# Performance work log

Hardware: AMD Instinct MI355X
Metric: run time of the kernel (lower is better)

Reference implementation:

```python
import jax, jax.numpy as jnp
import numpy as np

W_CHAMFER = 1.0
W_SMOOTH = 0.5
K_NEIGHBORS = 8


def _pairwise_sqdist(a, b):
    # a: [B,N,3], b: [B,M,3] -> [B,N,M] squared euclidean distances
    a2 = jnp.sum(a * a, axis=-1)  # [B,N]
    b2 = jnp.sum(b * b, axis=-1)  # [B,M]
    ab = jnp.einsum('bnd,bmd->bnm', a, b)  # [B,N,M]
    d2 = a2[:, :, None] + b2[:, None, :] - 2.0 * ab
    return jnp.maximum(d2, 0.0)


def _chamfer(pc1, pc2):
    d = jnp.sqrt(_pairwise_sqdist(pc1, pc2))  # [B,N,M] euclidean (matches torch.norm)
    d1 = jnp.min(d, axis=2)  # [B,N]
    d2 = jnp.min(d, axis=1)  # [B,M]
    return jnp.mean(d1) + jnp.mean(d2)


def _smoothness(pc, flow, k=K_NEIGHBORS):
    d2 = _pairwise_sqdist(pc, pc)  # [B,N,N]
    # k+1 nearest (squared dist preserves ordering); drop self (index 0)
    _, idx = jax.lax.top_k(-d2, k + 1)  # [B,N,k+1]
    idx = idx[:, :, 1:]  # [B,N,k]
    neighbor_flow = jax.vmap(lambda f, i: f[i])(flow, idx)  # [B,N,k,3]
    diff = flow[:, :, None, :] - neighbor_flow
    return jnp.mean(jnp.linalg.norm(diff, axis=-1))


def setup_inputs() -> dict:
    key = jax.random.key(0)
    k1, k2, k3 = jax.random.split(key, 3)
    B, N, M = 2, 8192, 8192
    pc1 = jax.random.normal(k1, (B, N, 3), dtype=jnp.float32)
    pc2 = jax.random.normal(k2, (B, M, 3), dtype=jnp.float32)
    pred_flow = jax.random.normal(k3, (B, N, 3), dtype=jnp.float32) * 0.1
    return {"pc1": pc1, "pc2": pc2, "pred_flow": pred_flow}


def reference(pc1, pc2, pred_flow):
    pc1_warped = pc1 + pred_flow
    l_chamfer = _chamfer(pc1_warped, pc2)
    l_smooth = _smoothness(pc1, pred_flow)
    return W_CHAMFER * l_chamfer + W_SMOOTH * l_smooth
```

## Files before the change

### kernel.cpp

```cpp
#include <hip/hip_runtime.h>

#define N_PTS 8192
#define BATCH 2
#define KNN 8
#define STILE 2048
#define PPB 16
#define CH_R 8
#define CH_SLICE 256

__device__ __forceinline__ void ce(unsigned &x, unsigned &y) {
    unsigned lo = min(x, y), hi = max(x, y); x = lo; y = hi;
}

__device__ __forceinline__ void insert4(unsigned o[4], unsigned key) {
    unsigned n0 = min(o[0], key);
    unsigned n1 = max(o[0], min(o[1], key));
    unsigned n2 = max(o[1], min(o[2], key));
    unsigned n3 = max(o[2], min(o[3], key));
    o[0]=n0; o[1]=n1; o[2]=n2; o[3]=n3;
}

__device__ __forceinline__ void merge_stage8(unsigned m[8], int d) {
    unsigned p[8], c[8];
    #pragma unroll
    for (int k = 0; k < 8; ++k) p[k] = __shfl_xor(m[k], d, 64);
    #pragma unroll
    for (int k = 0; k < 8; ++k) c[k] = min(m[k], p[7-k]);
    ce(c[0],c[4]); ce(c[1],c[5]); ce(c[2],c[6]); ce(c[3],c[7]);
    ce(c[0],c[2]); ce(c[1],c[3]); ce(c[4],c[6]); ce(c[5],c[7]);
    ce(c[0],c[1]); ce(c[2],c[3]); ce(c[4],c[5]); ce(c[6],c[7]);
    #pragma unroll
    for (int k = 0; k < 8; ++k) m[k] = c[k];
}

__device__ __forceinline__ void merge64(unsigned m[8]) {
    merge_stage8(m, 1); merge_stage8(m, 2); merge_stage8(m, 4);
    merge_stage8(m, 8); merge_stage8(m, 16); merge_stage8(m, 32);
}

__global__ void init_kernel(unsigned int* __restrict__ mins, float* __restrict__ out, int n) {
    int i = blockIdx.x * blockDim.x + threadIdx.x;
    if (i < n) mins[i] = 0x7F800000u;
    if (i == 0) out[0] = 0.0f;
}

__global__ __launch_bounds__(256, 4) void chamfer_min_kernel(const float* __restrict__ pc1,
                                                             const float* __restrict__ pc2,
                                                             const float* __restrict__ flow,
                                                             unsigned* __restrict__ mins) {
    const int z = blockIdx.z;
    const int b = z & 1, dir = z >> 1;
    const int tid = threadIdx.x;
    const float* base1 = pc1 + (size_t)b * N_PTS * 3;
    const float* base2 = pc2 + (size_t)b * N_PTS * 3;
    const float* fl    = flow + (size_t)b * N_PTS * 3;

    __shared__ float  sraw[CH_SLICE * 3];
    __shared__ float4 sq[CH_SLICE];
    const int m0 = blockIdx.y * CH_SLICE;

    if (tid < CH_SLICE * 3 / 4) {
        float4 v;
        if (dir == 0) {
            v = ((const float4*)(base2 + (size_t)m0 * 3))[tid];
        } else {
            float4 a = ((const float4*)(base1 + (size_t)m0 * 3))[tid];
            float4 f = ((const float4*)(fl    + (size_t)m0 * 3))[tid];
            v = make_float4(a.x + f.x, a.y + f.y, a.z + f.z, a.w + f.w);
        }
        ((float4*)sraw)[tid] = v;
    }

    const int i0 = blockIdx.x * (256 * CH_R) + tid * CH_R;
    float mx[CH_R], my_[CH_R], mz_[CH_R], p2[CH_R], best[CH_R];
    #pragma unroll
    for (int r = 0; r < CH_R; ++r) {
        int row = i0 + r;
        float px, py, pz;
        if (dir == 0) {
            px = base1[row*3+0] + fl[row*3+0];
            py = base1[row*3+1] + fl[row*3+1];
            pz = base1[row*3+2] + fl[row*3+2];
        } else {
            px = base2[row*3+0]; py = base2[row*3+1]; pz = base2[row*3+2];
        }
        mx[r] = -2.0f * px; my_[r] = -2.0f * py; mz_[r] = -2.0f * pz;
        p2[r] = fmaf(px, px, fmaf(py, py, pz * pz));
        best[r] = __builtin_inff();
    }
    __syncthreads();
    {
        float qx = sraw[tid*3+0], qy = sraw[tid*3+1], qz = sraw[tid*3+2];
        sq[tid] = make_float4(qx, qy, qz, fmaf(qx, qx, fmaf(qy, qy, qz * qz)));
    }
    __syncthreads();

    #pragma unroll 1
    for (int g = 0; g < CH_SLICE; g += 8) {
        float4 q[8];
        #pragma unroll
        for (int u = 0; u < 8; ++u) q[u] = sq[g + u];
        #pragma unroll
        for (int u = 0; u < 8; ++u) {
            #pragma unroll
            for (int r = 0; r < CH_R; ++r) {
                float s = fmaf(mx[r], q[u].x, fmaf(my_[r], q[u].y, fmaf(mz_[r], q[u].z, q[u].w)));
                best[r] = fminf(best[r], s);
            }
        }
    }
    #pragma unroll
    for (int r = 0; r < CH_R; ++r) {
        float d2 = fmaxf(best[r] + p2[r], 0.0f);
        atomicMin(&mins[((size_t)dir * BATCH + b) * N_PTS + i0 + r], __float_as_uint(d2));
    }
}

__global__ void chamfer_reduce_kernel(const unsigned int* __restrict__ mins,
                                      float* __restrict__ out) {
    int i = blockIdx.x * 256 + threadIdx.x;
    float v = sqrtf(__uint_as_float(mins[i])) * (1.0f / (float)(BATCH * N_PTS));
    #pragma unroll
    for (int off = 32; off > 0; off >>= 1) v += __shfl_down(v, off, 64);
    __shared__ float wsum[4];
    int wid = threadIdx.x >> 6;
    if ((threadIdx.x & 63) == 0) wsum[wid] = v;
    __syncthreads();
    if (threadIdx.x == 0) {
        atomicAdd(out, wsum[0] + wsum[1] + wsum[2] + wsum[3]);
    }
}

__global__ __launch_bounds__(256, 4) void smooth_kernel(const float* __restrict__ pc1,
                                                        const float* __restrict__ flow,
                                                        float* __restrict__ out) {
    const int b = blockIdx.y;
    const int tid = threadIdx.x;
    const int wv = tid >> 6, lane = tid & 63;
    const int i0w = blockIdx.x * PPB + wv * 4;
    const float* P = pc1  + (size_t)b * N_PTS * 3;
    const float* F = flow + (size_t)b * N_PTS * 3;

    float mx[4], my[4], mz[4], p2[4], gr[4];
    #pragma unroll
    for (int r = 0; r < 4; ++r) {
        int i = i0w + r;
        float px = P[i*3+0], py = P[i*3+1], pz = P[i*3+2];
        mx[r] = -2.0f * px; my[r] = -2.0f * py; mz[r] = -2.0f * pz;
        p2[r] = fmaf(px, px, fmaf(py, py, pz * pz));
        gr[r] = __builtin_inff();
    }

    unsigned o[4][4];
    #pragma unroll
    for (int r = 0; r < 4; ++r) {
        #pragma unroll
        for (int k = 0; k < 4; ++k) o[r][k] = 0xFFFFFFFFu;
    }

    __shared__ float4 sq[STILE];
    __shared__ float psum[4];

    #pragma unroll 1
    for (int tile = 0; tile < N_PTS / STILE; ++tile) {
        const int t0 = tile * STILE;
        __syncthreads();
        for (int u = tid; u < STILE; u += 256) {
            int g = t0 + u;
            float qx = P[g*3+0], qy = P[g*3+1], qz = P[g*3+2];
            sq[u] = make_float4(qx, qy, qz, fmaf(qx, qx, fmaf(qy, qy, qz * qz)));
        }
        __syncthreads();

        if (tile == 0) {
            float4 qa = sq[lane];
            #pragma unroll 1
            for (int st = 0; st < 32; ++st) {
                float4 qb = sq[(((st + 1) & 31) * 64) + lane];
                int j = st * 64 + lane;
                #pragma unroll
                for (int r = 0; r < 4; ++r) {
                    float s = fmaf(mx[r], qa.x, fmaf(my[r], qa.y, fmaf(mz[r], qa.z, qa.w)));
                    float d2 = fmaxf(s + p2[r], 0.0f);
                    unsigned key = (__float_as_uint(d2) & 0xFFFFE000u) | (unsigned)j;
                    key = (j == i0w + r) ? 0xFFFFFFFFu : key;
                    insert4(o[r], key);
                }
                qa = qb;
            }
            #pragma unroll
            for (int r = 0; r < 4; ++r) {
                unsigned m[8] = {o[r][0], o[r][1], o[r][2], o[r][3],
                                 0xFFFFFFFFu, 0xFFFFFFFFu, 0xFFFFFFFFu, 0xFFFFFFFFu};
                merge64(m);
                float thr_up = __uint_as_float((m[7] & 0xFFFFE000u) + 0x4000u);
                gr[r] = thr_up - p2[r];
            }
        } else {
            float4 qa = sq[lane];
            #pragma unroll 1
            for (int st = 0; st < 32; ++st) {
                float4 qb = sq[(((st + 1) & 31) * 64) + lane];
                int j = t0 + st * 64 + lane;
                float s0 = fmaf(mx[0], qa.x, fmaf(my[0], qa.y, fmaf(mz[0], qa.z, qa.w)));
                float s1 = fmaf(mx[1], qa.x, fmaf(my[1], qa.y, fmaf(mz[1], qa.z, qa.w)));
                float s2 = fmaf(mx[2], qa.x, fmaf(my[2], qa.y, fmaf(mz[2], qa.z, qa.w)));
                float s3 = fmaf(mx[3], qa.x, fmaf(my[3], qa.y, fmaf(mz[3], qa.z, qa.w)));
                if (__any(s0 <= gr[0])) {
                    float d2 = fmaxf(s0 + p2[0], 0.0f);
                    unsigned key = (__float_as_uint(d2) & 0xFFFFE000u) | (unsigned)j;
                    key = (j == i0w + 0) ? 0xFFFFFFFFu : key;
                    insert4(o[0], key);
                }
                if (__any(s1 <= gr[1])) {
                    float d2 = fmaxf(s1 + p2[1], 0.0f);
                    unsigned key = (__float_as_uint(d2) & 0xFFFFE000u) | (unsigned)j;
                    key = (j == i0w + 1) ? 0xFFFFFFFFu : key;
                    insert4(o[1], key);
                }
                if (__any(s2 <= gr[2])) {
                    float d2 = fmaxf(s2 + p2[2], 0.0f);
                    unsigned key = (__float_as_uint(d2) & 0xFFFFE000u) | (unsigned)j;
                    key = (j == i0w + 2) ? 0xFFFFFFFFu : key;
                    insert4(o[2], key);
                }
                if (__any(s3 <= gr[3])) {
                    float d2 = fmaxf(s3 + p2[3], 0.0f);
                    unsigned key = (__float_as_uint(d2) & 0xFFFFE000u) | (unsigned)j;
                    key = (j == i0w + 3) ? 0xFFFFFFFFu : key;
                    insert4(o[3], key);
                }
                qa = qb;
            }
        }
    }

    unsigned fin[4][8];
    #pragma unroll
    for (int r = 0; r < 4; ++r) {
        unsigned m[8] = {o[r][0], o[r][1], o[r][2], o[r][3],
                         0xFFFFFFFFu, 0xFFFFFFFFu, 0xFFFFFFFFu, 0xFFFFFFFFu};
        merge64(m);
        #pragma unroll
        for (int k = 0; k < 8; ++k) fin[r][k] = m[k];
    }

    const int sel = lane & 31;
    unsigned key = fin[0][0];
    #pragma unroll
    for (int rr = 0; rr < 4; ++rr) {
        #pragma unroll
        for (int kk = 0; kk < 8; ++kk) {
            if (sel == rr * 8 + kk) key = fin[rr][kk];
        }
    }
    const int r = sel >> 3;
    const int i = i0w + r;
    const int j = (int)(key & (N_PTS - 1));
    float dx = F[i*3+0] - F[j*3+0];
    float dy = F[i*3+1] - F[j*3+1];
    float dz = F[i*3+2] - F[j*3+2];
    float s = sqrtf(fmaf(dx, dx, fmaf(dy, dy, dz * dz)));
    #pragma unroll
    for (int d = 1; d < 64; d <<= 1) s += __shfl_xor(s, d, 64);
    if (lane == 0) psum[wv] = s;
    __syncthreads();
    if (tid == 0) {
        atomicAdd(out, (psum[0] + psum[1] + psum[2] + psum[3]) *
                       (0.25f / ((float)BATCH * N_PTS * KNN)));
    }
}

extern "C" void kernel_launch(void* const* d_in, const int* in_sizes, int n_in,
                              void* d_out, int out_size, void* d_ws, size_t ws_size,
                              hipStream_t stream) {
    const float* pc1  = (const float*)d_in[0];
    const float* pc2  = (const float*)d_in[1];
    const float* flow = (const float*)d_in[2];
    float* out = (float*)d_out;
    unsigned int* mins = (unsigned int*)d_ws;

    init_kernel<<<dim3(128), 256, 0, stream>>>(mins, out, 2 * BATCH * N_PTS);

    dim3 gch(N_PTS / (256 * CH_R), N_PTS / CH_SLICE, 2 * BATCH);
    chamfer_min_kernel<<<gch, 256, 0, stream>>>(pc1, pc2, flow, mins);

    chamfer_reduce_kernel<<<dim3(2 * BATCH * N_PTS / 256), 256, 0, stream>>>(mins, out);

    smooth_kernel<<<dim3(N_PTS / PPB, BATCH), 256, 0, stream>>>(pc1, flow, out);
}
```

Baseline: 161.1 us.

## Fuse chamfer and smoothness kernels into one launch with partial-min stores

Merges the chamfer nearest-distance blocks and the kNN smoothness blocks into a single grid, so both phases run concurrently and launch gaps go away. Chamfer partial minima are written to a per-slice workspace array and reduced in the finishing kernel, replacing atomicMin when the workspace is large enough. The init kernel is replaced by memsets. The smoothness pruning threshold is now tightened after each of the first three tiles using a cheap wave-wide reduction instead of a full merge after tile 0. This adds a larger workspace footprint and a heavier reduce pass, and mixing two very different block types in one grid may cause load imbalance.

```diff
diff --git a/kernel.cpp b/kernel.cpp
--- a/kernel.cpp
+++ b/kernel.cpp
@@ -7,6 +7,11 @@
 #define PPB 16
 #define CH_R 8
 #define CH_SLICE 256
+#define NSLICE (N_PTS / CH_SLICE)
+#define CH_BLOCKS 512
+#define SM_BLOCKS (N_PTS / PPB * BATCH)
+#define WS_STORE_NEED (4 * 1024 * 1024)
+#define OFF_MINS 0
 
 __device__ __forceinline__ void ce(unsigned &x, unsigned &y) {
     unsigned lo = min(x, y), hi = max(x, y); x = lo; y = hi;
@@ -38,237 +43,247 @@
     merge_stage8(m, 8); merge_stage8(m, 16); merge_stage8(m, 32);
 }
 
-__global__ void init_kernel(unsigned int* __restrict__ mins, float* __restrict__ out, int n) {
-    int i = blockIdx.x * blockDim.x + threadIdx.x;
-    if (i < n) mins[i] = 0x7F800000u;
-    if (i == 0) out[0] = 0.0f;
-}
-
-__global__ __launch_bounds__(256, 4) void chamfer_min_kernel(const float* __restrict__ pc1,
-                                                             const float* __restrict__ pc2,
-                                                             const float* __restrict__ flow,
-                                                             unsigned* __restrict__ mins) {
-    const int z = blockIdx.z;
-    const int b = z & 1, dir = z >> 1;
+__global__ __launch_bounds__(256, 4) void mega_kernel(
+        const float* __restrict__ pc1, const float* __restrict__ pc2,
+        const float* __restrict__ flow, float* __restrict__ part,
+        unsigned* __restrict__ mins, float* __restrict__ out, int store_mode) {
+    __shared__ float4 sq[STILE];
     const int tid = threadIdx.x;
-    const float* base1 = pc1 + (size_t)b * N_PTS * 3;
-    const float* base2 = pc2 + (size_t)b * N_PTS * 3;
-    const float* fl    = flow + (size_t)b * N_PTS * 3;
-
-    __shared__ float  sraw[CH_SLICE * 3];
-    __shared__ float4 sq[CH_SLICE];
-    const int m0 = blockIdx.y * CH_SLICE;
-
-    if (tid < CH_SLICE * 3 / 4) {
-        float4 v;
-        if (dir == 0) {
-            v = ((const float4*)(base2 + (size_t)m0 * 3))[tid];
+    const int bx = blockIdx.x;
+
+    if (bx < CH_BLOCKS) {
+        const int rt    = bx & 3;
+        const int slice = (bx >> 2) & 31;
+        const int z     = bx >> 7;
+        const int b = z & 1, dir = z >> 1;
+        const float* P1 = pc1  + (size_t)b * N_PTS * 3;
+        const float* P2 = pc2  + (size_t)b * N_PTS * 3;
+        const float* FL = flow + (size_t)b * N_PTS * 3;
+        const int m0 = slice * CH_SLICE;
+
+        float* sraw = (float*)(sq + 256);
+        if (tid < CH_SLICE * 3 / 4) {
+            float4 v;
+            if (dir == 0) {
+                v = ((const float4*)(P2 + (size_t)m0 * 3))[tid];
+            } else {
+                float4 a = ((const float4*)(P1 + (size_t)m0 * 3))[tid];
+                float4 f = ((const float4*)(FL + (size_t)m0 * 3))[tid];
+                v = make_float4(a.x + f.x, a.y + f.y, a.z + f.z, a.w + f.w);
+            }
+            ((float4*)sraw)[tid] = v;
+        }
+
+        const int i0 = rt * (256 * CH_R) + tid * CH_R;
+        float mx[CH_R], my_[CH_R], mz_[CH_R], p2[CH_R], best[CH_R];
+        #pragma unroll
+        for (int r = 0; r < CH_R; ++r) {
+            int row = i0 + r;
+            float px, py, pz;
+            if (dir == 0) {
+                px = P1[row*3+0] + FL[row*3+0];
+                py = P1[row*3+1] + FL[row*3+1];
+                pz = P1[row*3+2] + FL[row*3+2];
+            } else {
+                px = P2[row*3+0]; py = P2[row*3+1]; pz = P2[row*3+2];
+            }
+            mx[r] = -2.0f * px; my_[r] = -2.0f * py; mz_[r] = -2.0f * pz;
+            p2[r] = fmaf(px, px, fmaf(py, py, pz * pz));
+            best[r] = __builtin_inff();
+        }
+        __syncthreads();
+        {
+            float qx = sraw[tid*3+0], qy = sraw[tid*3+1], qz = sraw[tid*3+2];
+            sq[tid] = make_float4(qx, qy, qz, fmaf(qx, qx, fmaf(qy, qy, qz * qz)));
+        }
+        __syncthreads();
+
+        #pragma unroll 8
+        for (int jj = 0; jj < CH_SLICE; ++jj) {
+            float4 q = sq[jj];
+            #pragma unroll
+            for (int r = 0; r < CH_R; ++r) {
+                float s = fmaf(mx[r], q.x, fmaf(my_[r], q.y, fmaf(mz_[r], q.z, q.w)));
+                best[r] = fminf(best[r], s);
+            }
+        }
+
+        float d2v[CH_R];
+        #pragma unroll
+        for (int r = 0; r < CH_R; ++r) d2v[r] = fmaxf(best[r] + p2[r], 0.0f);
+        if (store_mode) {
+            float* dst = part + ((size_t)(z * NSLICE + slice)) * N_PTS + i0;
+            *(float4*)(dst)     = make_float4(d2v[0], d2v[1], d2v[2], d2v[3]);
+            *(float4*)(dst + 4) = make_float4(d2v[4], d2v[5], d2v[6], d2v[7]);
         } else {
-            float4 a = ((const float4*)(base1 + (size_t)m0 * 3))[tid];
-            float4 f = ((const float4*)(fl    + (size_t)m0 * 3))[tid];
-            v = make_float4(a.x + f.x, a.y + f.y, a.z + f.z, a.w + f.w);
-        }
-        ((float4*)sraw)[tid] = v;
+            #pragma unroll
+            for (int r = 0; r < CH_R; ++r)
+                atomicMin(&mins[z * N_PTS + i0 + r], __float_as_uint(d2v[r]));
+        }
+    } else {
+        const int s  = bx - CH_BLOCKS;
+        const int b  = s >> 9;
+        const int sx = s & 511;
+        const int wv = tid >> 6, lane = tid & 63;
+        const int i0w = sx * PPB + wv * 4;
+        const float* P = pc1  + (size_t)b * N_PTS * 3;
+        const float* F = flow + (size_t)b * N_PTS * 3;
+
+        float mx[4], my[4], mz[4], p2[4], gr[4];
+        unsigned thr[4];
+        #pragma unroll
+        for (int r = 0; r < 4; ++r) {
+            int i = i0w + r;
+            float px = P[i*3+0], py = P[i*3+1], pz = P[i*3+2];
+            mx[r] = -2.0f * px; my[r] = -2.0f * py; mz[r] = -2.0f * pz;
+            p2[r] = fmaf(px, px, fmaf(py, py, pz * pz));
+            gr[r] = __builtin_inff();
+            thr[r] = 0xFFFFFFFFu;
+        }
+
+        unsigned o[4][4];
+        #pragma unroll
+        for (int r = 0; r < 4; ++r)
+            #pragma unroll
+            for (int k = 0; k < 4; ++k) o[r][k] = 0xFFFFFFFFu;
+
+        __shared__ float psum[4];
+
+        #pragma unroll 1
+        for (int tile = 0; tile < N_PTS / STILE; ++tile) {
+            const int t0 = tile * STILE;
+            __syncthreads();
+            #pragma unroll
+            for (int u = tid; u < STILE; u += 256) {
+                int g = t0 + u;
+                float qx = P[g*3+0], qy = P[g*3+1], qz = P[g*3+2];
+                sq[u] = make_float4(qx, qy, qz, fmaf(qx, qx, fmaf(qy, qy, qz * qz)));
+            }
+            __syncthreads();
+
+            if (tile == 0) {
+                #pragma unroll 4
+                for (int st = 0; st < STILE / 64; ++st) {
+                    float4 qa = sq[st * 64 + lane];
+                    int j = st * 64 + lane;
+                    #pragma unroll
+                    for (int r = 0; r < 4; ++r) {
+                        float ss = fmaf(mx[r], qa.x, fmaf(my[r], qa.y, fmaf(mz[r], qa.z, qa.w)));
+                        float d2 = fmaxf(ss + p2[r], 0.0f);
+                        unsigned key = (__float_as_uint(d2) & 0xFFFFE000u) | (unsigned)j;
+                        key = (j == i0w + r) ? 0xFFFFFFFFu : key;
+                        insert4(o[r], key);
+                    }
+                }
+            } else {
+                #pragma unroll 4
+                for (int st = 0; st < STILE / 64; ++st) {
+                    float4 qa = sq[st * 64 + lane];
+                    int j = t0 + st * 64 + lane;
+                    float s0 = fmaf(mx[0], qa.x, fmaf(my[0], qa.y, fmaf(mz[0], qa.z, qa.w)));
+                    float s1 = fmaf(mx[1], qa.x, fmaf(my[1], qa.y, fmaf(mz[1], qa.z, qa.w)));
+                    float s2 = fmaf(mx[2], qa.x, fmaf(my[2], qa.y, fmaf(mz[2], qa.z, qa.w)));
+                    float s3 = fmaf(mx[3], qa.x, fmaf(my[3], qa.y, fmaf(mz[3], qa.z, qa.w)));
+                    if (__any(s0 <= gr[0])) {
+                        float d2 = fmaxf(s0 + p2[0], 0.0f);
+                        unsigned key = (__float_as_uint(d2) & 0xFFFFE000u) | (unsigned)j;
+                        key = (j == i0w + 0) ? 0xFFFFFFFFu : key;
+                        insert4(o[0], key);
+                    }
+                    if (__any(s1 <= gr[1])) {
+                        float d2 = fmaxf(s1 + p2[1], 0.0f);
+                        unsigned key = (__float_as_uint(d2) & 0xFFFFE000u) | (unsigned)j;
+                        key = (j == i0w + 1) ? 0xFFFFFFFFu : key;
+                        insert4(o[1], key);
+                    }
+                    if (__any(s2 <= gr[2])) {
+                        float d2 = fmaxf(s2 + p2[2], 0.0f);
+                        unsigned key = (__float_as_uint(d2) & 0xFFFFE000u) | (unsigned)j;
+                        key = (j == i0w + 2) ? 0xFFFFFFFFu : key;
+                        insert4(o[2], key);
+                    }
+                    if (__any(s3 <= gr[3])) {
+                        float d2 = fmaxf(s3 + p2[3], 0.0f);
+                        unsigned key = (__float_as_uint(d2) & 0xFFFFE000u) | (unsigned)j;
+                        key = (j == i0w + 3) ? 0xFFFFFFFFu : key;
+                        insert4(o[3], key);
+                    }
+                }
+            }
+
+            if (tile <= 2) {
+                #pragma unroll
+                for (int r = 0; r < 4; ++r) {
+                    unsigned a = max(o[r][3], (unsigned)__shfl_xor((int)o[r][3], 1, 64));
+                    a = min(a, (unsigned)__shfl_xor((int)a, 2, 64));
+                    a = min(a, (unsigned)__shfl_xor((int)a, 4, 64));
+                    a = min(a, (unsigned)__shfl_xor((int)a, 8, 64));
+                    a = min(a, (unsigned)__shfl_xor((int)a, 16, 64));
+                    a = min(a, (unsigned)__shfl_xor((int)a, 32, 64));
+                    thr[r] = min(thr[r], a);
+                    float thr_up = __uint_as_float((thr[r] & 0xFFFFE000u) + 0x4000u);
+                    gr[r] = thr_up - p2[r];
+                }
+            }
+        }
+
+        unsigned fin[4][8];
+        #pragma unroll
+        for (int r = 0; r < 4; ++r) {
+            unsigned m[8] = {o[r][0], o[r][1], o[r][2], o[r][3],
+                             0xFFFFFFFFu, 0xFFFFFFFFu, 0xFFFFFFFFu, 0xFFFFFFFFu};
+            merge64(m);
+            #pragma unroll
+            for (int k = 0; k < 8; ++k) fin[r][k] = m[k];
+        }
+
+        const int sel = lane & 31;
+        unsigned key = fin[0][0];
+        #pragma unroll
+        for (int rr = 0; rr < 4; ++rr)
+            #pragma unroll
+            for (int kk = 0; kk < 8; ++kk)
+                if (sel == rr * 8 + kk) key = fin[rr][kk];
+        const int r = sel >> 3;
+        const int i = i0w + r;
+        const int j = (int)(key & (N_PTS - 1));
+        float dx = F[i*3+0] - F[j*3+0];
+        float dy = F[i*3+1] - F[j*3+1];
+        float dz = F[i*3+2] - F[j*3+2];
+        float sv = sqrtf(fmaf(dx, dx, fmaf(dy, dy, dz * dz)));
+        #pragma unroll
+        for (int d = 1; d < 64; d <<= 1) sv += __shfl_xor(sv, d, 64);
+        if (lane == 0) psum[wv] = sv;
+        __syncthreads();
+        if (tid == 0) {
+            atomicAdd(out, (psum[0] + psum[1] + psum[2] + psum[3]) *
+                           (0.25f / ((float)BATCH * N_PTS * KNN)));
+        }
     }
-
-    const int i0 = blockIdx.x * (256 * CH_R) + tid * CH_R;
-    float mx[CH_R], my_[CH_R], mz_[CH_R], p2[CH_R], best[CH_R];
+}
+
+__global__ void chamfer_reduce_kernel(const unsigned* __restrict__ mins,
+                                      const float* __restrict__ part,
+                                      float* __restrict__ out, int store_mode) {
+    int t = blockIdx.x * 256 + threadIdx.x;
+    float v;
+    if (store_mode) {
+        int c = t >> 13, row = t & (N_PTS - 1);
+        const float* p = part + ((size_t)c * NSLICE) * N_PTS + row;
+        v = __builtin_inff();
+        #pragma unroll 8
+        for (int s = 0; s < NSLICE; ++s) v = fminf(v, p[(size_t)s * N_PTS]);
+    } else {
+        v = __uint_as_float(mins[t]);
+    }
+    float d = sqrtf(v) * (1.0f / (float)(BATCH * N_PTS));
     #pragma unroll
-    for (int r = 0; r < CH_R; ++r) {
-        int row = i0 + r;
-        float px, py, pz;
-        if (dir == 0) {
-            px = base1[row*3+0] + fl[row*3+0];
-            py = base1[row*3+1] + fl[row*3+1];
-            pz = base1[row*3+2] + fl[row*3+2];
-        } else {
-            px = base2[row*3+0]; py = base2[row*3+1]; pz = base2[row*3+2];
-        }
-        mx[r] = -2.0f * px; my_[r] = -2.0f * py; mz_[r] = -2.0f * pz;
-        p2[r] = fmaf(px, px, fmaf(py, py, pz * pz));
-        best[r] = __builtin_inff();
-    }
-    __syncthreads();
-    {
-        float qx = sraw[tid*3+0], qy = sraw[tid*3+1], qz = sraw[tid*3+2];
-        sq[tid] = make_float4(qx, qy, qz, fmaf(qx, qx, fmaf(qy, qy, qz * qz)));
-    }
-    __syncthreads();
-
-    #pragma unroll 1
-    for (int g = 0; g < CH_SLICE; g += 8) {
-        float4 q[8];
-        #pragma unroll
-        for (int u = 0; u < 8; ++u) q[u] = sq[g + u];
-        #pragma unroll
-        for (int u = 0; u < 8; ++u) {
-            #pragma unroll
-            for (int r = 0; r < CH_R; ++r) {
-                float s = fmaf(mx[r], q[u].x, fmaf(my_[r], q[u].y, fmaf(mz_[r], q[u].z, q[u].w)));
-                best[r] = fminf(best[r], s);
-            }
-        }
-    }
-    #pragma unroll
-    for (int r = 0; r < CH_R; ++r) {
-        float d2 = fmaxf(best[r] + p2[r], 0.0f);
-        atomicMin(&mins[((size_t)dir * BATCH + b) * N_PTS + i0 + r], __float_as_uint(d2));
-    }
-}
-
-__global__ void chamfer_reduce_kernel(const unsigned int* __restrict__ mins,
-                                      float* __restrict__ out) {
-    int i = blockIdx.x * 256 + threadIdx.x;
-    float v = sqrtf(__uint_as_float(mins[i])) * (1.0f / (float)(BATCH * N_PTS));
-    #pragma unroll
-    for (int off = 32; off > 0; off >>= 1) v += __shfl_down(v, off, 64);
+    for (int off = 32; off > 0; off >>= 1) d += __shfl_down(d, off, 64);
     __shared__ float wsum[4];
     int wid = threadIdx.x >> 6;
-    if ((threadIdx.x & 63) == 0) wsum[wid] = v;
+    if ((threadIdx.x & 63) == 0) wsum[wid] = d;
     __syncthreads();
-    if (threadIdx.x == 0) {
-        atomicAdd(out, wsum[0] + wsum[1] + wsum[2] + wsum[3]);
-    }
-}
-
-__global__ __launch_bounds__(256, 4) void smooth_kernel(const float* __restrict__ pc1,
-                                                        const float* __restrict__ flow,
-                                                        float* __restrict__ out) {
-    const int b = blockIdx.y;
-    const int tid = threadIdx.x;
-    const int wv = tid >> 6, lane = tid & 63;
-    const int i0w = blockIdx.x * PPB + wv * 4;
-    const float* P = pc1  + (size_t)b * N_PTS * 3;
-    const float* F = flow + (size_t)b * N_PTS * 3;
-
-    float mx[4], my[4], mz[4], p2[4], gr[4];
-    #pragma unroll
-    for (int r = 0; r < 4; ++r) {
-        int i = i0w + r;
-        float px = P[i*3+0], py = P[i*3+1], pz = P[i*3+2];
-        mx[r] = -2.0f * px; my[r] = -2.0f * py; mz[r] = -2.0f * pz;
-        p2[r] = fmaf(px, px, fmaf(py, py, pz * pz));
-        gr[r] = __builtin_inff();
-    }
-
-    unsigned o[4][4];
-    #pragma unroll
-    for (int r = 0; r < 4; ++r) {
-        #pragma unroll
-        for (int k = 0; k < 4; ++k) o[r][k] = 0xFFFFFFFFu;
-    }
-
-    __shared__ float4 sq[STILE];
-    __shared__ float psum[4];
-
-    #pragma unroll 1
-    for (int tile = 0; tile < N_PTS / STILE; ++tile) {
-        const int t0 = tile * STILE;
-        __syncthreads();
-        for (int u = tid; u < STILE; u += 256) {
-            int g = t0 + u;
-            float qx = P[g*3+0], qy = P[g*3+1], qz = P[g*3+2];
-            sq[u] = make_float4(qx, qy, qz, fmaf(qx, qx, fmaf(qy, qy, qz * qz)));
-        }
-        __syncthreads();
-
-        if (tile == 0) {
-            float4 qa = sq[lane];
-            #pragma unroll 1
-            for (int st = 0; st < 32; ++st) {
-                float4 qb = sq[(((st + 1) & 31) * 64) + lane];
-                int j = st * 64 + lane;
-                #pragma unroll
-                for (int r = 0; r < 4; ++r) {
-                    float s = fmaf(mx[r], qa.x, fmaf(my[r], qa.y, fmaf(mz[r], qa.z, qa.w)));
-                    float d2 = fmaxf(s + p2[r], 0.0f);
-                    unsigned key = (__float_as_uint(d2) & 0xFFFFE000u) | (unsigned)j;
-                    key = (j == i0w + r) ? 0xFFFFFFFFu : key;
-                    insert4(o[r], key);
-                }
-                qa = qb;
-            }
-            #pragma unroll
-            for (int r = 0; r < 4; ++r) {
-                unsigned m[8] = {o[r][0], o[r][1], o[r][2], o[r][3],
-                                 0xFFFFFFFFu, 0xFFFFFFFFu, 0xFFFFFFFFu, 0xFFFFFFFFu};
-                merge64(m);
-                float thr_up = __uint_as_float((m[7] & 0xFFFFE000u) + 0x4000u);
-                gr[r] = thr_up - p2[r];
-            }
-        } else {
-            float4 qa = sq[lane];
-            #pragma unroll 1
-            for (int st = 0; st < 32; ++st) {
-                float4 qb = sq[(((st + 1) & 31) * 64) + lane];
-                int j = t0 + st * 64 + lane;
-                float s0 = fmaf(mx[0], qa.x, fmaf(my[0], qa.y, fmaf(mz[0], qa.z, qa.w)));
-                float s1 = fmaf(mx[1], qa.x, fmaf(my[1], qa.y, fmaf(mz[1], qa.z, qa.w)));
-                float s2 = fmaf(mx[2], qa.x, fmaf(my[2], qa.y, fmaf(mz[2], qa.z, qa.w)));
-                float s3 = fmaf(mx[3], qa.x, fmaf(my[3], qa.y, fmaf(mz[3], qa.z, qa.w)));
-                if (__any(s0 <= gr[0])) {
-                    float d2 = fmaxf(s0 + p2[0], 0.0f);
-                    unsigned key = (__float_as_uint(d2) & 0xFFFFE000u) | (unsigned)j;
-                    key = (j == i0w + 0) ? 0xFFFFFFFFu : key;
-                    insert4(o[0], key);
-                }
-                if (__any(s1 <= gr[1])) {
-                    float d2 = fmaxf(s1 + p2[1], 0.0f);
-                    unsigned key = (__float_as_uint(d2) & 0xFFFFE000u) | (unsigned)j;
-                    key = (j == i0w + 1) ? 0xFFFFFFFFu : key;
-                    insert4(o[1], key);
-                }
-                if (__any(s2 <= gr[2])) {
-                    float d2 = fmaxf(s2 + p2[2], 0.0f);
-                    unsigned key = (__float_as_uint(d2) & 0xFFFFE000u) | (unsigned)j;
-                    key = (j == i0w + 2) ? 0xFFFFFFFFu : key;
-                    insert4(o[2], key);
-                }
-                if (__any(s3 <= gr[3])) {
-                    float d2 = fmaxf(s3 + p2[3], 0.0f);
-                    unsigned key = (__float_as_uint(d2) & 0xFFFFE000u) | (unsigned)j;
-                    key = (j == i0w + 3) ? 0xFFFFFFFFu : key;
-                    insert4(o[3], key);
-                }
-                qa = qb;
-            }
-        }
-    }
-
-    unsigned fin[4][8];
-    #pragma unroll
-    for (int r = 0; r < 4; ++r) {
-        unsigned m[8] = {o[r][0], o[r][1], o[r][2], o[r][3],
-                         0xFFFFFFFFu, 0xFFFFFFFFu, 0xFFFFFFFFu, 0xFFFFFFFFu};
-        merge64(m);
-        #pragma unroll
-        for (int k = 0; k < 8; ++k) fin[r][k] = m[k];
-    }
-
-    const int sel = lane & 31;
-    unsigned key = fin[0][0];
-    #pragma unroll
-    for (int rr = 0; rr < 4; ++rr) {
-        #pragma unroll
-        for (int kk = 0; kk < 8; ++kk) {
-            if (sel == rr * 8 + kk) key = fin[rr][kk];
-        }
-    }
-    const int r = sel >> 3;
-    const int i = i0w + r;
-    const int j = (int)(key & (N_PTS - 1));
-    float dx = F[i*3+0] - F[j*3+0];
-    float dy = F[i*3+1] - F[j*3+1];
-    float dz = F[i*3+2] - F[j*3+2];
-    float s = sqrtf(fmaf(dx, dx, fmaf(dy, dy, dz * dz)));
-    #pragma unroll
-    for (int d = 1; d < 64; d <<= 1) s += __shfl_xor(s, d, 64);
-    if (lane == 0) psum[wv] = s;
-    __syncthreads();
-    if (tid == 0) {
-        atomicAdd(out, (psum[0] + psum[1] + psum[2] + psum[3]) *
-                       (0.25f / ((float)BATCH * N_PTS * KNN)));
-    }
+    if (threadIdx.x == 0) atomicAdd(out, wsum[0] + wsum[1] + wsum[2] + wsum[3]);
 }
 
 extern "C" void kernel_launch(void* const* d_in, const int* in_sizes, int n_in,
@@ -278,14 +293,19 @@
     const float* pc2  = (const float*)d_in[1];
     const float* flow = (const float*)d_in[2];
     float* out = (float*)d_out;
-    unsigned int* mins = (unsigned int*)d_ws;
-
-    init_kernel<<<dim3(128), 256, 0, stream>>>(mins, out, 2 * BATCH * N_PTS);
-
-    dim3 gch(N_PTS / (256 * CH_R), N_PTS / CH_SLICE, 2 * BATCH);
-    chamfer_min_kernel<<<gch, 256, 0, stream>>>(pc1, pc2, flow, mins);
-
-    chamfer_reduce_kernel<<<dim3(2 * BATCH * N_PTS / 256), 256, 0, stream>>>(mins, out);
-
-    smooth_kernel<<<dim3(N_PTS / PPB, BATCH), 256, 0, stream>>>(pc1, flow, out);
-}
+    float* part = (float*)d_ws;
+    unsigned* mins = (unsigned*)((char*)d_ws + OFF_MINS);
+
+    const int store_mode = (ws_size >= (size_t)WS_STORE_NEED) ? 1 : 0;
+
+    hipMemsetAsync(out, 0, sizeof(float), stream);
+    if (!store_mode) {
+        hipMemsetAsync(mins, 0xFF, 4u * N_PTS * sizeof(unsigned), stream);
+    }
+
+    mega_kernel<<<dim3(CH_BLOCKS + SM_BLOCKS), 256, 0, stream>>>(
+        pc1, pc2, flow, part, mins, out, store_mode);
+
+    chamfer_reduce_kernel<<<dim3(2 * BATCH * N_PTS / 256), 256, 0, stream>>>(
+        mins, part, out, store_mode);
+}
```

Result: faster. 151.9 us (-5.7%).
